# Performance work log

Hardware: AMD Instinct MI355X
Metric: run time of the kernel (lower is better)

## Reference

```python
import jax, jax.numpy as jnp
import numpy as np

B, H, S, D = 2, 16, 2048, 128
EPS = 1e-12  # F.normalize default eps
NEG = -1000000000.0


def setup_inputs() -> dict:
    key = jax.random.key(0)
    kq, kk, kv, km = jax.random.split(key, 4)
    q = jax.random.normal(kq, (B, H, S, D), dtype=jnp.float32)
    k = jax.random.normal(kk, (B, H, S, D), dtype=jnp.float32)
    v = jax.random.normal(kv, (B, H, S, D), dtype=jnp.float32)
    mask = jax.random.randint(km, (B, 1, 1, S), 0, 2).astype(jnp.int32)
    return {"q": q, "k": k, "v": v, "mask": mask}


def reference(q, k, v, mask):
    # L2-normalize k along dim=1 (the HEAD axis), matching F.normalize(k, p=2, dim=1)
    k_norm = k / jnp.maximum(jnp.linalg.norm(k, axis=1, keepdims=True), EPS)
    # attn scores: [B,H,S,S]
    attn = jnp.einsum('bhqd,bhkd->bhqk', q, k_norm)
    attn = jnp.where(mask == 0, NEG, attn)
    attn = jax.nn.softmax(attn, axis=-1)
    # dropout is identity in eval mode (deterministic reference)
    out = jnp.einsum('bhqk,bhkd->bhqd', attn, v)
    return (out, attn)
```

## Files before the change

kernel.cpp:

```cpp
#include <hip/hip_runtime.h>
#include <hip/hip_fp16.h>

#define BB 2
#define HH 16
#define SS 2048
#define DD 128
#define CHUNK 64
#define NCHUNK 32
#define QBLK 32
#define CSHIFT 14.0f

typedef __attribute__((ext_vector_type(8))) _Float16 f16x8;
typedef __attribute__((ext_vector_type(4))) _Float16 f16x4;
typedef __attribute__((ext_vector_type(4))) float    f32x4;

__device__ __forceinline__ void load_lds16(const void* g, void* l) {
  __builtin_amdgcn_global_load_lds(
      (const __attribute__((address_space(1))) void*)g,
      (__attribute__((address_space(3))) void*)l, 16, 0, 0);
}

__device__ __forceinline__ void block_barrier() {
  asm volatile("" ::: "memory");
  __builtin_amdgcn_s_barrier();
  asm volatile("" ::: "memory");
}

__global__ void knorm_f16(const float* __restrict__ k, _Float16* __restrict__ kh) {
  int t = blockIdx.x * 256 + threadIdx.x;
  int d = t & (DD - 1);
  int s = (t >> 7) & (SS - 1);
  int b = t >> 18;
  const float* kp = k + (size_t)b * HH * SS * DD + (size_t)s * DD + d;
  float vals[HH];
  float ss = 0.f;
  #pragma unroll
  for (int h = 0; h < HH; ++h) { float x = kp[(size_t)h * SS * DD]; vals[h] = x; ss += x * x; }
  float r = 1.0f / fmaxf(sqrtf(ss), 1e-12f);
  const int doff = (((d >> 3) ^ (s & 7)) << 3) + (d & 7);
  _Float16* op = kh + (size_t)b * HH * SS * DD + (size_t)s * DD + doff;
  #pragma unroll
  for (int h = 0; h < HH; ++h) op[(size_t)h * SS * DD] = (_Float16)(vals[h] * r);
}

__global__ void cvt_f16(const float* __restrict__ x, _Float16* __restrict__ y) {
  size_t i = ((size_t)blockIdx.x * 256 + threadIdx.x) * 8;
  float4 a = *(const float4*)(x + i);
  float4 b = *(const float4*)(x + i + 4);
  f16x8 r = { (_Float16)a.x, (_Float16)a.y, (_Float16)a.z, (_Float16)a.w,
              (_Float16)b.x, (_Float16)b.y, (_Float16)b.z, (_Float16)b.w };
  *(f16x8*)(y + i) = r;
}

__global__ void vtrans_f16(const float* __restrict__ v, _Float16* __restrict__ vt) {
  __shared__ float tile[32][33];
  int bh = blockIdx.z;
  int d0 = blockIdx.x * 32, s0 = blockIdx.y * 32;
  const float* vp = v + (size_t)bh * SS * DD;
  _Float16* tp = vt + (size_t)bh * SS * DD;
  int tx = threadIdx.x, ty = threadIdx.y;
  #pragma unroll
  for (int i = ty; i < 32; i += 8)
    tile[i][tx] = vp[(size_t)(s0 + i) * DD + d0 + tx];
  __syncthreads();
  #pragma unroll
  for (int i = ty; i < 32; i += 8) {
    const int key = s0 + tx, dd = d0 + i;
    tp[(size_t)(key >> 6) * (DD * CHUNK) + (size_t)dd * CHUNK
       + ((((key & 63) >> 3) ^ (dd & 7)) << 3) + (key & 7)] = (_Float16)tile[tx][i];
  }
}

__global__ __launch_bounds__(512, 4) void attn_fused(
    const _Float16* __restrict__ qh, const _Float16* __restrict__ kh,
    const _Float16* __restrict__ vth, const int* __restrict__ mask,
    float* __restrict__ out, float* __restrict__ attn)
{
  __shared__ _Float16 kbuf[2][CHUNK * DD];
  __shared__ _Float16 vbuf[2][DD * CHUNK];
  __shared__ _Float16 pbuf[QBLK * CHUNK];
  __shared__ float redsum[2][16][5];

  const int wgid = blockIdx.x;
  const int xcd  = wgid & 7;
  const int idx  = wgid >> 3;
  const int bh   = (xcd << 2) | (idx >> 6);
  const int q0   = (idx & 63) * QBLK;
  const int b    = bh >> 4;

  const int tid  = threadIdx.x;
  const int lane = tid & 63;
  const int w    = tid >> 6;
  const int lo16 = lane & 15;
  const int g    = lane >> 4;
  const int qhf  = w >> 2;
  const int sub  = w & 3;

  const size_t hoff = (size_t)bh * SS * DD;
  const _Float16* Q = qh  + hoff + (size_t)q0 * DD;
  const _Float16* K = kh  + hoff;
  const _Float16* V = vth + hoff;
  const int* mrow = mask + b * SS;

  const int prow = qhf * 16 + lo16;

  f16x8 qf[4];
  #pragma unroll
  for (int c = 0; c < 4; ++c)
    qf[c] = *(const f16x8*)(Q + (size_t)prow * DD + c * 32 + g * 8);

  #pragma unroll
  for (int j = 0; j < 2; ++j) {
    const int slot = tid + j * 512;
    load_lds16(K + slot * 8, &kbuf[0][slot * 8]);
    load_lds16(V + slot * 8, &vbuf[0][slot * 8]);
  }
  __syncthreads();

  f16x4 acc_h[NCHUNK];
  f32x4 oacc[2] = { {0,0,0,0}, {0,0,0,0} };
  float ssum = 0.f;

  #pragma unroll
  for (int c = 0; c < NCHUNK; ++c) {
    const _Float16* kb = kbuf[c & 1];
    const _Float16* vb = vbuf[c & 1];

    if (c + 1 < NCHUNK) {
      #pragma unroll
      for (int j = 0; j < 2; ++j) {
        const int slot = tid + j * 512;
        load_lds16(K + (size_t)(c + 1) * (CHUNK * DD) + slot * 8,
                   &kbuf[(c + 1) & 1][slot * 8]);
        load_lds16(V + (size_t)(c + 1) * (CHUNK * DD) + slot * 8,
                   &vbuf[(c + 1) & 1][slot * 8]);
      }
    }

    {
      const int row = sub * 16 + lo16;
      f32x4 a = {0.f, 0.f, 0.f, 0.f};
      #pragma unroll
      for (int cc = 0; cc < 4; ++cc) {
        const int p = (cc * 4 + g) ^ (row & 7);
        f16x8 kf = *(const f16x8*)(kb + row * DD + p * 8);
        a = __builtin_amdgcn_mfma_f32_16x16x32_f16(kf, qf[cc], a, 0, 0, 0);
      }
      const int4 mv = *(const int4*)(mrow + c * CHUNK + sub * 16 + g * 4);
      const float e0 = mv.x ? __expf(a[0] - CSHIFT) : 0.f;
      const float e1 = mv.y ? __expf(a[1] - CSHIFT) : 0.f;
      const float e2 = mv.z ? __expf(a[2] - CSHIFT) : 0.f;
      const float e3 = mv.w ? __expf(a[3] - CSHIFT) : 0.f;
      ssum += e0 + e1 + e2 + e3;
      f16x4 eh = { (_Float16)e0, (_Float16)e1, (_Float16)e2, (_Float16)e3 };
      acc_h[c] = eh;
      const int col = sub * 16 + g * 4;
      *(f16x4*)(&pbuf[prow * CHUNK + (((col >> 3) ^ (prow & 7)) << 3) + (col & 7)]) = eh;
    }
    asm volatile("s_waitcnt lgkmcnt(0)" ::: "memory");
    block_barrier();

    {
      #pragma unroll
      for (int t = 0; t < 2; ++t) {
        const int dcol = sub * 32 + t * 16 + lo16;
        #pragma unroll
        for (int ks = 0; ks < 2; ++ks) {
          const int pv_ = (ks * 4 + g) ^ (dcol & 7);
          f16x8 vf = *(const f16x8*)(vb + dcol * CHUNK + pv_ * 8);
          f16x8 pf = *(const f16x8*)(&pbuf[prow * CHUNK + ((ks * 32 + g * 8) ^ ((prow & 7) << 3))]);
          oacc[t] = __builtin_amdgcn_mfma_f32_16x16x32_f16(pf, vf, oacc[t], 0, 0, 0);
        }
      }
    }
    asm volatile("s_waitcnt vmcnt(0)" ::: "memory");
    block_barrier();
  }

  ssum += __shfl_xor(ssum, 16);
  ssum += __shfl_xor(ssum, 32);
  if (lane < 16) redsum[qhf][lane][sub] = ssum;
  __syncthreads();

  float denom = 0.f;
  #pragma unroll
  for (int j = 0; j < 4; ++j) denom += redsum[qhf][lo16][j];
  const float inv = 1.0f / denom;

  float* arow = attn + ((size_t)bh * SS + q0 + prow) * SS + sub * 16 + g * 4;
  #pragma unroll
  for (int c = 0; c < NCHUNK; ++c) {
    f32x4 pst = { (float)acc_h[c][0] * inv, (float)acc_h[c][1] * inv,
                  (float)acc_h[c][2] * inv, (float)acc_h[c][3] * inv };
    *(f32x4*)(arow + c * CHUNK) = pst;
  }

  float* O = out + hoff + (size_t)q0 * DD + sub * 32;
  #pragma unroll
  for (int i = 0; i < 4; ++i) {
    const int qr = g * 4 + i;
    float dq = 0.f;
    #pragma unroll
    for (int j = 0; j < 4; ++j) dq += redsum[qhf][qr][j];
    const float rdq = 1.0f / dq;
    #pragma unroll
    for (int t = 0; t < 2; ++t)
      O[(size_t)(qhf * 16 + qr) * DD + t * 16 + lo16] = oacc[t][i] * rdq;
  }
}

extern "C" void kernel_launch(void* const* d_in, const int* in_sizes, int n_in,
                              void* d_out, int out_size, void* d_ws, size_t ws_size,
                              hipStream_t stream) {
  const float* q    = (const float*)d_in[0];
  const float* k    = (const float*)d_in[1];
  const float* v    = (const float*)d_in[2];
  const int*   mask = (const int*)d_in[3];

  const size_t N = (size_t)BB * HH * SS * DD;
  float* out  = (float*)d_out;
  float* attn = out + N;

  _Float16* qh  = (_Float16*)d_ws;
  _Float16* kh  = qh + N;
  _Float16* vth = kh + N;

  cvt_f16  <<<N / 8 / 256, 256, 0, stream>>>(q, qh);
  knorm_f16<<<(BB * SS * DD) / 256, 256, 0, stream>>>(k, kh);
  vtrans_f16<<<dim3(DD / 32, SS / 32, BB * HH), dim3(32, 8), 0, stream>>>(v, vth);

  attn_fused<<<2048, 512, 0, stream>>>(qh, kh, vth, mask, out, attn);
}
```

Baseline: 313.8 us.

## Read V directly from global and software-pipeline PV one chunk behind QK

V is now stored as a plain transposed [D][S] fp16 layout and read straight from global memory into registers instead of being staged through LDS. The P tile is double-buffered so the PV matmul for chunk c-1 runs in the same iteration as the QK/softmax for chunk c, which removes one block barrier per iteration. This halves LDS staging traffic and barriers, but V loads now come uncoalesced-ish from global/L2 with latency exposed at the MFMA, and the global load waits are merged into one vmcnt(0) per iteration.

```diff
diff --git a/kernel.cpp b/kernel.cpp
--- a/kernel.cpp
+++ b/kernel.cpp
@@ -5,8 +5,8 @@
 #define HH 16
 #define SS 2048
 #define DD 128
-#define CHUNK 64
-#define NCHUNK 32
+#define CH 64
+#define NCH 32
 #define QBLK 32
 #define CSHIFT 14.0f
 
@@ -64,11 +64,8 @@
     tile[i][tx] = vp[(size_t)(s0 + i) * DD + d0 + tx];
   __syncthreads();
   #pragma unroll
-  for (int i = ty; i < 32; i += 8) {
-    const int key = s0 + tx, dd = d0 + i;
-    tp[(size_t)(key >> 6) * (DD * CHUNK) + (size_t)dd * CHUNK
-       + ((((key & 63) >> 3) ^ (dd & 7)) << 3) + (key & 7)] = (_Float16)tile[tx][i];
-  }
+  for (int i = ty; i < 32; i += 8)
+    tp[(size_t)(d0 + i) * SS + s0 + tx] = (_Float16)tile[tx][i];
 }
 
 __global__ __launch_bounds__(512, 4) void attn_fused(
@@ -76,9 +73,8 @@
     const _Float16* __restrict__ vth, const int* __restrict__ mask,
     float* __restrict__ out, float* __restrict__ attn)
 {
-  __shared__ _Float16 kbuf[2][CHUNK * DD];
-  __shared__ _Float16 vbuf[2][DD * CHUNK];
-  __shared__ _Float16 pbuf[QBLK * CHUNK];
+  __shared__ _Float16 kbuf[2][CH * DD];
+  __shared__ _Float16 pbuf[2][QBLK * CH];
   __shared__ float redsum[2][16][5];
 
   const int wgid = blockIdx.x;
@@ -113,27 +109,23 @@
   for (int j = 0; j < 2; ++j) {
     const int slot = tid + j * 512;
     load_lds16(K + slot * 8, &kbuf[0][slot * 8]);
-    load_lds16(V + slot * 8, &vbuf[0][slot * 8]);
   }
   __syncthreads();
 
-  f16x4 acc_h[NCHUNK];
+  f16x4 acc_h[NCH];
   f32x4 oacc[2] = { {0,0,0,0}, {0,0,0,0} };
   float ssum = 0.f;
 
   #pragma unroll
-  for (int c = 0; c < NCHUNK; ++c) {
+  for (int c = 0; c < NCH; ++c) {
     const _Float16* kb = kbuf[c & 1];
-    const _Float16* vb = vbuf[c & 1];
-
-    if (c + 1 < NCHUNK) {
+
+    if (c + 1 < NCH) {
       #pragma unroll
       for (int j = 0; j < 2; ++j) {
         const int slot = tid + j * 512;
-        load_lds16(K + (size_t)(c + 1) * (CHUNK * DD) + slot * 8,
+        load_lds16(K + (size_t)(c + 1) * (CH * DD) + slot * 8,
                    &kbuf[(c + 1) & 1][slot * 8]);
-        load_lds16(V + (size_t)(c + 1) * (CHUNK * DD) + slot * 8,
-                   &vbuf[(c + 1) & 1][slot * 8]);
       }
     }
 
@@ -146,7 +138,7 @@
         f16x8 kf = *(const f16x8*)(kb + row * DD + p * 8);
         a = __builtin_amdgcn_mfma_f32_16x16x32_f16(kf, qf[cc], a, 0, 0, 0);
       }
-      const int4 mv = *(const int4*)(mrow + c * CHUNK + sub * 16 + g * 4);
+      const int4 mv = *(const int4*)(mrow + c * CH + sub * 16 + g * 4);
       const float e0 = mv.x ? __expf(a[0] - CSHIFT) : 0.f;
       const float e1 = mv.y ? __expf(a[1] - CSHIFT) : 0.f;
       const float e2 = mv.z ? __expf(a[2] - CSHIFT) : 0.f;
@@ -155,26 +147,42 @@
       f16x4 eh = { (_Float16)e0, (_Float16)e1, (_Float16)e2, (_Float16)e3 };
       acc_h[c] = eh;
       const int col = sub * 16 + g * 4;
-      *(f16x4*)(&pbuf[prow * CHUNK + (((col >> 3) ^ (prow & 7)) << 3) + (col & 7)]) = eh;
-    }
-    asm volatile("s_waitcnt lgkmcnt(0)" ::: "memory");
-    block_barrier();
-
-    {
+      *(f16x4*)(&pbuf[c & 1][prow * CH + (((col >> 3) ^ (prow & 7)) << 3) + (col & 7)]) = eh;
+    }
+
+    if (c > 0) {
+      const int kc = (c - 1) * CH;
       #pragma unroll
       for (int t = 0; t < 2; ++t) {
         const int dcol = sub * 32 + t * 16 + lo16;
         #pragma unroll
         for (int ks = 0; ks < 2; ++ks) {
-          const int pv_ = (ks * 4 + g) ^ (dcol & 7);
-          f16x8 vf = *(const f16x8*)(vb + dcol * CHUNK + pv_ * 8);
-          f16x8 pf = *(const f16x8*)(&pbuf[prow * CHUNK + ((ks * 32 + g * 8) ^ ((prow & 7) << 3))]);
+          f16x8 vf = *(const f16x8*)(V + (size_t)dcol * SS + kc + ks * 32 + g * 8);
+          f16x8 pf = *(const f16x8*)(&pbuf[(c - 1) & 1]
+                       [prow * CH + ((ks * 32 + g * 8) ^ ((prow & 7) << 3))]);
           oacc[t] = __builtin_amdgcn_mfma_f32_16x16x32_f16(pf, vf, oacc[t], 0, 0, 0);
         }
       }
     }
-    asm volatile("s_waitcnt vmcnt(0)" ::: "memory");
+
+    asm volatile("s_waitcnt lgkmcnt(0)" ::: "memory");
+    asm volatile("s_waitcnt vmcnt(0)"  ::: "memory");
     block_barrier();
+  }
+
+  {
+    const int kc = (NCH - 1) * CH;
+    #pragma unroll
+    for (int t = 0; t < 2; ++t) {
+      const int dcol = sub * 32 + t * 16 + lo16;
+      #pragma unroll
+      for (int ks = 0; ks < 2; ++ks) {
+        f16x8 vf = *(const f16x8*)(V + (size_t)dcol * SS + kc + ks * 32 + g * 8);
+        f16x8 pf = *(const f16x8*)(&pbuf[(NCH - 1) & 1]
+                     [prow * CH + ((ks * 32 + g * 8) ^ ((prow & 7) << 3))]);
+        oacc[t] = __builtin_amdgcn_mfma_f32_16x16x32_f16(pf, vf, oacc[t], 0, 0, 0);
+      }
+    }
   }
 
   ssum += __shfl_xor(ssum, 16);
@@ -189,10 +197,10 @@
 
   float* arow = attn + ((size_t)bh * SS + q0 + prow) * SS + sub * 16 + g * 4;
   #pragma unroll
-  for (int c = 0; c < NCHUNK; ++c) {
+  for (int c = 0; c < NCH; ++c) {
     f32x4 pst = { (float)acc_h[c][0] * inv, (float)acc_h[c][1] * inv,
                   (float)acc_h[c][2] * inv, (float)acc_h[c][3] * inv };
-    *(f32x4*)(arow + c * CHUNK) = pst;
+    *(f32x4*)(arow + c * CH) = pst;
   }
 
   float* O = out + hoff + (size_t)q0 * DD + sub * 32;
```

New measurement: 477.6 us. +52.2%, slower.
